# Optimization experiments

Measured on AMD Instinct MI355X. Metric: run time of the kernel, lower is better.

Reference implementation:

```python
import jax, jax.numpy as jnp
import numpy as np

EPS = 1e-05


def setup_inputs() -> dict:
    key = jax.random.key(0)
    k1, k2, k3, k4 = jax.random.split(key, 4)
    B, N, L, J = 1, 256, 192, 32
    n_feat_out = 128
    d2 = J * J  # 1024
    x_down = jax.random.normal(k1, (B, N, L, J), dtype=jnp.float32)
    x_down_w = jax.random.normal(k2, (B, N, L, J), dtype=jnp.float32)
    a_2 = jnp.ones((d2,), dtype=jnp.float32)
    b_2 = jnp.zeros((d2,), dtype=jnp.float32)
    # nn.Linear default init: U(-1/sqrt(fan_in), 1/sqrt(fan_in))
    bound = 1.0 / np.sqrt(d2)
    W = jax.random.uniform(k3, (d2, n_feat_out), dtype=jnp.float32, minval=-bound, maxval=bound)
    b = jax.random.uniform(k4, (n_feat_out,), dtype=jnp.float32, minval=-bound, maxval=bound)
    return {"x_down": x_down, "x_down_w": x_down_w, "a_2": a_2, "b_2": b_2, "W": W, "b": b}


def reference(x_down, x_down_w, a_2, b_2, W, b):
    B, N, L, J = x_down.shape
    # outer-product contraction over MSA dim: (B,L,L,J,J)
    pair = jnp.einsum('bnij,bnlm->biljm', x_down, x_down_w)
    pair = pair.reshape(B, L, L, J * J)
    # LayerNorm over last dim (biased variance, matching torch unbiased=False)
    mean = pair.mean(axis=-1, keepdims=True)
    var = pair.var(axis=-1, keepdims=True)
    pair = a_2 * (pair - mean) / jnp.sqrt(var + EPS) + b_2
    # Linear projection J^2 -> n_feat_out
    return pair @ W + b
```

## Files before the change

kernel.cpp:

```cpp
#include <hip/hip_runtime.h>
#include <hip/hip_bf16.h>
#include <stdint.h>

#define NN   256
#define LL   192
#define MDIM 6144
#define D2   1024
#define FF   128

typedef __bf16 bf16x8 __attribute__((ext_vector_type(8)));
typedef float  f32x4  __attribute__((ext_vector_type(4)));

#define MFMA16(a, b, c) __builtin_amdgcn_mfma_f32_16x16x32_bf16(a, b, c, 0, 0, 0)

__device__ __forceinline__ void gload_lds16(const void* g, void* l) {
  __builtin_amdgcn_global_load_lds(
      (__attribute__((address_space(1))) void*)(g),
      (__attribute__((address_space(3))) void*)(l),
      16, 0, 0);
}

static __device__ __forceinline__ unsigned short bf16_bits(float v) {
  __bf16 h = (__bf16)v;
  return __builtin_bit_cast(unsigned short, h);
}

__global__ __launch_bounds__(256)
void prep_all(const float* __restrict__ x1, const float* __restrict__ x2,
              const float* __restrict__ W, const float* __restrict__ a2,
              const float* __restrict__ b2, const float* __restrict__ bias,
              __bf16* __restrict__ At, __bf16* __restrict__ Bt,
              __bf16* __restrict__ WB, float* __restrict__ S,
              float* __restrict__ T) {
  __shared__ float tile[32][33];
  const int b = blockIdx.x;
  const int t = threadIdx.x;
  if (b < 3072) {
    const float* src = (b < 1536) ? x1 : x2;
    __bf16* dst = (b < 1536) ? At : Bt;
    const int bb = (b < 1536) ? b : b - 1536;
    const int m0 = (bb % 192) * 32;
    const int k0 = (bb / 192) * 32;
    {
      const int kr = t >> 3, mc = (t & 7) * 4;
      const float4 v = *(const float4*)&src[(size_t)(k0 + kr) * MDIM + m0 + mc];
      tile[kr][mc + 0] = v.x;
      tile[kr][mc + 1] = v.y;
      tile[kr][mc + 2] = v.z;
      tile[kr][mc + 3] = v.w;
    }
    __syncthreads();
    {
      const int mr = t >> 3, kc = (t & 7) * 4;
      ushort4 u;
      u.x = bf16_bits(tile[kc + 0][mr]);
      u.y = bf16_bits(tile[kc + 1][mr]);
      u.z = bf16_bits(tile[kc + 2][mr]);
      u.w = bf16_bits(tile[kc + 3][mr]);
      *(ushort4*)&dst[(size_t)(m0 + mr) * NN + k0 + kc] = u;
    }
  } else {
    const int f = b - 3072;
    float s = 0.f, tt = 0.f;
#pragma unroll
    for (int it = 0; it < 4; ++it) {
      const int k = t + it * 256;
      const float wv = W[(size_t)k * FF + f];
      const __bf16 wa = (__bf16)(a2[k] * wv);
      WB[(size_t)(k >> 5) * 4096 + f * 32 + ((k >> 3) & 3) * 8 + (k & 7)] = wa;
      s += (float)wa;
      tt += b2[k] * wv;
    }
#pragma unroll
    for (int off = 32; off; off >>= 1) {
      s += __shfl_xor(s, off);
      tt += __shfl_xor(tt, off);
    }
    const int wv_ = t >> 6, ln = t & 63;
    if (ln == 0) { tile[0][wv_] = s; tile[1][wv_] = tt; }
    __syncthreads();
    if (t == 0) {
      S[f] = tile[0][0] + tile[0][1] + tile[0][2] + tile[0][3];
      T[f] = tile[1][0] + tile[1][1] + tile[1][2] + tile[1][3] + bias[f];
    }
  }
}

__global__ __launch_bounds__(256)
void fused4(const __bf16* __restrict__ At, const __bf16* __restrict__ Bt,
            const __bf16* __restrict__ WB, const float* __restrict__ S,
            const float* __restrict__ T, float* __restrict__ out) {
  __shared__ uint8_t lds[32768];
  __shared__ float mean_s[16], rstd_s[16];

  const int tid = threadIdx.x;
  const int w = tid >> 6;
  const int lane = tid & 63;
  const int q = lane >> 4;
  const int c = lane & 15;

  const int b = blockIdx.x;
  const int xcd = b & 7;
  const int s_ = b >> 3;
  const int bx = (xcd >> 1) * 12 + (s_ % 12);
  const int by = (xcd & 1) * 24 + (s_ / 12);
  const int m0 = bx * 128, n0 = by * 128;

  uint8_t* As = lds;
  uint8_t* Bs = lds + 16384;

  const int l8 = lane & 7;
  const int r8 = lane >> 3;
  const int gsw = l8 ^ r8;

  f32x4 acc[4][4];
#pragma unroll
  for (int i = 0; i < 4; ++i)
#pragma unroll
    for (int j = 0; j < 4; ++j)
      acc[i][j] = (f32x4){0.f, 0.f, 0.f, 0.f};

  const int mbase = (w & 1) * 64;
  const int nbase = (w >> 1) * 64;

  for (int kb = 0; kb < 4; ++kb) {
    __syncthreads();
#pragma unroll
    for (int s4 = 0; s4 < 4; ++s4) {
      const int mrow = s4 * 32 + w * 8 + r8;
      const uint8_t* ga = (const uint8_t*)At +
          (((size_t)(m0 + mrow)) * NN + kb * 64 + gsw * 8) * 2;
      const uint8_t* gb = (const uint8_t*)Bt +
          (((size_t)(n0 + mrow)) * NN + kb * 64 + gsw * 8) * 2;
      gload_lds16(ga, As + (s4 * 32 + w * 8) * 128);
      gload_lds16(gb, Bs + (s4 * 32 + w * 8) * 128);
    }
    __syncthreads();
#pragma unroll
    for (int ks = 0; ks < 2; ++ks) {
      bf16x8 a[4], bfr[4];
#pragma unroll
      for (int t4 = 0; t4 < 4; ++t4) {
        const int mr = mbase + t4 * 16 + c;
        const int slot = (ks * 4 + q) ^ (lane & 7);
        a[t4] = *(const bf16x8*)(As + mr * 128 + slot * 16);
        const int nr = nbase + t4 * 16 + c;
        bfr[t4] = *(const bf16x8*)(Bs + nr * 128 + slot * 16);
      }
#pragma unroll
      for (int ti = 0; ti < 4; ++ti)
#pragma unroll
        for (int tj = 0; tj < 4; ++tj)
          acc[ti][tj] = MFMA16(a[ti], bfr[tj], acc[ti][tj]);
    }
  }

  const int fb = w * 32;
  const __bf16* wb0 = WB + (fb + c) * 32 + q * 8;
  const __bf16* wb1 = WB + (fb + 16 + c) * 32 + q * 8;
  bf16x8 pb0[4], pb1[4];
#pragma unroll
  for (int p = 0; p < 4; ++p) {
    pb0[p] = *(const bf16x8*)(wb0 + p * 4096);
    pb1[p] = *(const bf16x8*)(wb1 + p * 4096);
  }

  __syncthreads();

  const int i_hi = w & 1, l_hi = w >> 1;
#pragma unroll
  for (int ab = 0; ab < 2; ++ab) {
#pragma unroll
    for (int cb = 0; cb < 2; ++cb) {
      float s1 = 0.f, s2 = 0.f;
#pragma unroll
      for (int dti = 0; dti < 2; ++dti)
#pragma unroll
        for (int dtj = 0; dtj < 2; ++dtj)
#pragma unroll
          for (int reg = 0; reg < 4; ++reg) {
            const float v = acc[ab * 2 + dti][cb * 2 + dtj][reg];
            s1 += v; s2 += v * v;
          }
#pragma unroll
      for (int off = 32; off; off >>= 1) {
        s1 += __shfl_xor(s1, off);
        s2 += __shfl_xor(s2, off);
      }
      const float mean = s1 * (1.0f / 1024.0f);
      const float var = s2 * (1.0f / 1024.0f) - mean * mean;
      const float rstd = rsqrtf(var + 1e-5f);
      const int r = (i_hi * 2 + ab) * 4 + (l_hi * 2 + cb);
      if (lane == 0) { mean_s[r] = mean; rstd_s[r] = rstd; }
      const int r7 = r & 7;
#pragma unroll
      for (int dti = 0; dti < 2; ++dti)
#pragma unroll
        for (int dtj = 0; dtj < 2; ++dtj)
#pragma unroll
          for (int rp = 0; rp < 4; rp += 2) {
            const float x = acc[ab * 2 + dti][cb * 2 + dtj][rp];
            const float y = acc[ab * 2 + dti][cb * 2 + dtj][rp + 1];
            const float send = (c & 1) ? x : y;
            const float recv = __shfl_xor(send, 1);
            const float vlo = (c & 1) ? recv : x;
            const float vhi = (c & 1) ? y : recv;
            const int reg_w = (c & 1) ? rp + 1 : rp;
            const int j = dti * 16 + q * 4 + reg_w;
            const int mm0 = dtj * 16 + (c & ~1);
            const int k = j * 32 + mm0;
            const int g = k >> 3;
            const int G = g ^ (g >> 4) ^ r7;
            const uint32_t dw =
                ((uint32_t)bf16_bits(vhi) << 16) | (uint32_t)bf16_bits(vlo);
            *(uint32_t*)(lds + r * 2048 + G * 16 + (mm0 & 7) * 2) = dw;
          }
    }
  }

  __syncthreads();

  f32x4 acc2[2];
  acc2[0] = (f32x4){0.f, 0.f, 0.f, 0.f};
  acc2[1] = (f32x4){0.f, 0.f, 0.f, 0.f};
  const int c7 = c & 7;
#pragma unroll
  for (int kstep = 0; kstep < 32; ++kstep) {
    const int g = kstep * 4 + q;
    const int G = g ^ (g >> 4) ^ c7;
    const bf16x8 av = *(const bf16x8*)(lds + c * 2048 + G * 16);
    acc2[0] = MFMA16(av, pb0[kstep & 3], acc2[0]);
    acc2[1] = MFMA16(av, pb1[kstep & 3], acc2[1]);
    if (kstep < 28) {
      pb0[kstep & 3] = *(const bf16x8*)(wb0 + (kstep + 4) * 4096);
      pb1[kstep & 3] = *(const bf16x8*)(wb1 + (kstep + 4) * 4096);
    }
  }

  const float S0 = S[fb + c], T0 = T[fb + c];
  const float S1 = S[fb + 16 + c], T1 = T[fb + 16 + c];
#pragma unroll
  for (int reg = 0; reg < 4; ++reg) {
    const int r = q * 4 + reg;
    const float mean = mean_s[r], rstd = rstd_s[r];
    const int i = bx * 4 + (r >> 2);
    const int l = by * 4 + (r & 3);
    const size_t base = ((size_t)i * LL + l) * FF;
    out[base + fb + c]      = rstd * (acc2[0][reg] - mean * S0) + T0;
    out[base + fb + 16 + c] = rstd * (acc2[1][reg] - mean * S1) + T1;
  }
}

extern "C" void kernel_launch(void* const* d_in, const int* in_sizes, int n_in,
                              void* d_out, int out_size, void* d_ws, size_t ws_size,
                              hipStream_t stream) {
  const float* x_down   = (const float*)d_in[0];
  const float* x_down_w = (const float*)d_in[1];
  const float* a2       = (const float*)d_in[2];
  const float* b2       = (const float*)d_in[3];
  const float* W        = (const float*)d_in[4];
  const float* bias     = (const float*)d_in[5];
  float* out = (float*)d_out;

  uint8_t* ws = (uint8_t*)d_ws;
  __bf16* At  = (__bf16*)(ws);
  __bf16* Bt  = (__bf16*)(ws + 3145728);
  __bf16* WB  = (__bf16*)(ws + 6291456);
  float*  S   = (float*)(ws + 6553600);
  float*  T   = (float*)(ws + 6554112);

  prep_all<<<dim3(3200), dim3(256), 0, stream>>>(x_down, x_down_w, W, a2, b2,
                                                 bias, At, Bt, WB, S, T);
  fused4<<<dim3(2304), dim3(256), 0, stream>>>(At, Bt, WB, S, T, out);
}
```

Measured before the change: 140.4 us.

## Double-buffer LDS staging in fused GEMM with 32-wide K steps

Restructures the main GEMM loop in the fused kernel to double-buffer the A and B tiles in LDS. The next K-slice's global-to-LDS loads are issued before computing on the current slice, so there is one barrier per step instead of two. The K slice shrinks from 64 to 32, so there are eight iterations. The XOR swizzle is dropped for a plain 64-byte row layout. Global latency should overlap with the MFMAs, but the unswizzled reads may cause LDS bank conflicts.

Result: no change. 142.6 us (+1.5%).

```diff
diff --git a/kernel.cpp b/kernel.cpp
--- a/kernel.cpp
+++ b/kernel.cpp
@@ -87,7 +87,7 @@
 }
 
 __global__ __launch_bounds__(256)
-void fused4(const __bf16* __restrict__ At, const __bf16* __restrict__ Bt,
+void fused5(const __bf16* __restrict__ At, const __bf16* __restrict__ Bt,
             const __bf16* __restrict__ WB, const float* __restrict__ S,
             const float* __restrict__ T, float* __restrict__ out) {
   __shared__ uint8_t lds[32768];
@@ -106,13 +106,6 @@
   const int by = (xcd & 1) * 24 + (s_ / 12);
   const int m0 = bx * 128, n0 = by * 128;
 
-  uint8_t* As = lds;
-  uint8_t* Bs = lds + 16384;
-
-  const int l8 = lane & 7;
-  const int r8 = lane >> 3;
-  const int gsw = l8 ^ r8;
-
   f32x4 acc[4][4];
 #pragma unroll
   for (int i = 0; i < 4; ++i)
@@ -123,37 +116,41 @@
   const int mbase = (w & 1) * 64;
   const int nbase = (w >> 1) * 64;
 
-  for (int kb = 0; kb < 4; ++kb) {
+  const int srow = w * 32 + (lane >> 2);
+  const int sgrp = lane & 3;
+
+#define STAGE(kb_, base_)                                                     \
+  do {                                                                        \
+    gload_lds16(At + (size_t)(m0 + srow) * NN + (kb_) * 32 + sgrp * 8,        \
+                (base_) + (w * 32) * 64);                                     \
+    gload_lds16(At + (size_t)(m0 + srow + 16) * NN + (kb_) * 32 + sgrp * 8,   \
+                (base_) + (w * 32 + 16) * 64);                                \
+    gload_lds16(Bt + (size_t)(n0 + srow) * NN + (kb_) * 32 + sgrp * 8,        \
+                (base_) + 8192 + (w * 32) * 64);                              \
+    gload_lds16(Bt + (size_t)(n0 + srow + 16) * NN + (kb_) * 32 + sgrp * 8,   \
+                (base_) + 8192 + (w * 32 + 16) * 64);                         \
+  } while (0)
+
+  STAGE(0, lds);
+#pragma unroll
+  for (int kb = 0; kb < 8; ++kb) {
+    uint8_t* cur = lds + (kb & 1) * 16384;
+    uint8_t* nxt = lds + ((kb + 1) & 1) * 16384;
     __syncthreads();
-#pragma unroll
-    for (int s4 = 0; s4 < 4; ++s4) {
-      const int mrow = s4 * 32 + w * 8 + r8;
-      const uint8_t* ga = (const uint8_t*)At +
-          (((size_t)(m0 + mrow)) * NN + kb * 64 + gsw * 8) * 2;
-      const uint8_t* gb = (const uint8_t*)Bt +
-          (((size_t)(n0 + mrow)) * NN + kb * 64 + gsw * 8) * 2;
-      gload_lds16(ga, As + (s4 * 32 + w * 8) * 128);
-      gload_lds16(gb, Bs + (s4 * 32 + w * 8) * 128);
-    }
-    __syncthreads();
-#pragma unroll
-    for (int ks = 0; ks < 2; ++ks) {
-      bf16x8 a[4], bfr[4];
-#pragma unroll
-      for (int t4 = 0; t4 < 4; ++t4) {
-        const int mr = mbase + t4 * 16 + c;
-        const int slot = (ks * 4 + q) ^ (lane & 7);
-        a[t4] = *(const bf16x8*)(As + mr * 128 + slot * 16);
-        const int nr = nbase + t4 * 16 + c;
-        bfr[t4] = *(const bf16x8*)(Bs + nr * 128 + slot * 16);
-      }
-#pragma unroll
-      for (int ti = 0; ti < 4; ++ti)
-#pragma unroll
-        for (int tj = 0; tj < 4; ++tj)
-          acc[ti][tj] = MFMA16(a[ti], bfr[tj], acc[ti][tj]);
-    }
-  }
+    if (kb < 7) STAGE(kb + 1, nxt);
+    bf16x8 a[4], bfr[4];
+#pragma unroll
+    for (int t4 = 0; t4 < 4; ++t4) {
+      a[t4]   = *(const bf16x8*)(cur + (mbase + t4 * 16 + c) * 64 + q * 16);
+      bfr[t4] = *(const bf16x8*)(cur + 8192 + (nbase + t4 * 16 + c) * 64 + q * 16);
+    }
+#pragma unroll
+    for (int ti = 0; ti < 4; ++ti)
+#pragma unroll
+      for (int tj = 0; tj < 4; ++tj)
+        acc[ti][tj] = MFMA16(a[ti], bfr[tj], acc[ti][tj]);
+  }
+#undef STAGE
 
   const int fb = w * 32;
   const __bf16* wb0 = WB + (fb + c) * 32 + q * 8;
@@ -271,5 +268,5 @@
 
   prep_all<<<dim3(3200), dim3(256), 0, stream>>>(x_down, x_down_w, W, a2, b2,
                                                  bias, At, Bt, WB, S, T);
-  fused4<<<dim3(2304), dim3(256), 0, stream>>>(At, Bt, WB, S, T, out);
-}
+  fused5<<<dim3(2304), dim3(256), 0, stream>>>(At, Bt, WB, S, T, out);
+}
```
